# Performance work log

Measured on AMD Instinct MI355X. Metric: run time of the kernel, lower is better.

The kernel has to match this reference:

```python
import jax, jax.numpy as jnp
import numpy as np

B, S, IN, OUT = 4, 512, 1024, 512
T, G, K, R = 16, 2, 4, 32  # tables, groups, cells, rank
OUTPUT_SCALE = 1.0 / np.sqrt(T * G).astype(np.float32)


def setup_inputs() -> dict:
    key = jax.random.key(0)
    k0, k1, k2, k3 = jax.random.split(key, 4)
    x = jax.random.normal(k0, (B, S, IN), dtype=jnp.float32)
    proj_w = jax.random.normal(k1, (R, IN), dtype=jnp.float32) / np.sqrt(IN)
    router_w = jax.random.normal(k2, (T, G, K, R), dtype=jnp.float32) / np.sqrt(R)
    router_b = jnp.zeros((T, G, K), dtype=jnp.float32)
    affine_w = jax.random.normal(k3, (T, G, K, R, OUT), dtype=jnp.float32) * 0.02
    affine_b = jnp.zeros((T, G, K, OUT), dtype=jnp.float32)
    return {"x": x, "proj_w": proj_w, "router_w": router_w, "router_b": router_b,
            "affine_w": affine_w, "affine_b": affine_b}


def reference(x, proj_w, router_w, router_b, affine_w, affine_b):
    # z: (B,S,R) low-rank projection
    z = jnp.einsum('bsi,ri->bsr', x, proj_w)
    # routing scores per (table, group, cell): (B,S,T,G,K)
    scores = jnp.einsum('bsr,tgkr->bstgk', z, router_w) + router_b
    # per-cell affine outputs: (B,S,T,G,K,O) -- dominant intermediate
    cell_values = jnp.einsum('bsr,tgkro->bstgko', z, affine_w) + affine_b
    # tropical (min-plus) winner selection: argmin over cells
    winner = jnp.argmin(scores, axis=-1)  # (B,S,T,G)
    idx = jnp.broadcast_to(winner[..., None, None],
                           winner.shape + (1, cell_values.shape[-1]))
    group_output = jnp.take_along_axis(cell_values, idx, axis=4)[..., 0, :]  # (B,S,T,G,O)
    # sum over groups then tables, apply output scaling
    output = group_output.sum(axis=(2, 3)) * OUTPUT_SCALE  # (B,S,O)
    return output
```

## Files before the change

kernel.cpp:

```cpp
#include <hip/hip_runtime.h>

#define NTOK 2048
#define IN_DIM 1024
#define OUT_DIM 512
#define RNK 32
#define TG_N 32
#define TGK_N 128
#define AWCOLS 4096
#define KD 4224
#define NKT 66
#define SCALE_F 0.17677669529663687f

typedef __attribute__((ext_vector_type(8))) short short8;
typedef __attribute__((ext_vector_type(4))) float float4v;

__device__ __forceinline__ unsigned short f2bf(float f) {
  union { float f; unsigned int u; } c; c.f = f;
  unsigned int u = c.u;
  u += 0x7fffu + ((u >> 16) & 1u);
  return (unsigned short)(u >> 16);
}

__global__ __launch_bounds__(256) void k_w2t(
    const float* __restrict__ aw, const float* __restrict__ ab,
    unsigned short* __restrict__ w2t) {
  __shared__ float tile[32][33];
  const int c0 = blockIdx.x * 32, o0 = blockIdx.y * 32;
  const int t = threadIdx.x;
  const int oo = t & 31, cc = t >> 5;
#pragma unroll
  for (int p = 0; p < 4; ++p) {
    int cidx = c0 + cc + p * 8;
    float v = (cidx < AWCOLS)
                  ? aw[(size_t)cidx * OUT_DIM + o0 + oo]
                  : ab[(size_t)(cidx - AWCOLS) * OUT_DIM + o0 + oo];
    tile[cc + p * 8][oo] = v;
  }
  __syncthreads();
  if (t < 128) {
    const int ol = t >> 2, ch = t & 3;
    union { short8 v; unsigned short u[8]; } pk;
#pragma unroll
    for (int j = 0; j < 8; ++j) pk.u[j] = f2bf(tile[ch * 8 + j][ol]);
    *(short8*)(w2t + (size_t)(o0 + ol) * KD + c0 + ch * 8) = pk.v;
  }
}

__global__ __launch_bounds__(256) void k_zwin(
    const float* __restrict__ x, const float* __restrict__ proj_w,
    const float* __restrict__ router_w, const float* __restrict__ router_b,
    unsigned short* __restrict__ zout, unsigned long long* __restrict__ wout) {
  const int tok2 = blockIdx.x * 2;
  const int t = threadIdx.x;
  __shared__ __align__(16) float zbuf[2][RNK];
  __shared__ float sc[2][TGK_N];
  __shared__ int winbuf[2][TG_N];

  const int r = t >> 3, c = t & 7;
  const float4* w4 = (const float4*)(proj_w + (size_t)r * IN_DIM);
  const float4* x0 = (const float4*)(x + (size_t)tok2 * IN_DIM);
  float a0 = 0.f, a1 = 0.f;
#pragma unroll
  for (int jj = 0; jj < 32; ++jj) {
    float4 wv = w4[jj * 8 + c];
    float4 xv0 = x0[jj * 8 + c];
    float4 xv1 = x0[256 + jj * 8 + c];
    a0 += xv0.x * wv.x + xv0.y * wv.y + xv0.z * wv.z + xv0.w * wv.w;
    a1 += xv1.x * wv.x + xv1.y * wv.y + xv1.z * wv.z + xv1.w * wv.w;
  }
  a0 += __shfl_xor(a0, 1); a0 += __shfl_xor(a0, 2); a0 += __shfl_xor(a0, 4);
  a1 += __shfl_xor(a1, 1); a1 += __shfl_xor(a1, 2); a1 += __shfl_xor(a1, 4);
  if (c == 0) { zbuf[0][r] = a0; zbuf[1][r] = a1; }
  __syncthreads();

  {
    const int cell = t & 127, tk = t >> 7;
    const float4* rw = (const float4*)(router_w + (size_t)cell * RNK);
    const float4* zb = (const float4*)(&zbuf[tk][0]);
    float s = router_b[cell];
#pragma unroll
    for (int j = 0; j < 8; ++j) {
      float4 a = rw[j]; float4 b = zb[j];
      s += a.x * b.x + a.y * b.y + a.z * b.z + a.w * b.w;
    }
    sc[tk][cell] = s;
  }
  __syncthreads();

  if (t < 64) {
    const int tk = t >> 5, tg = t & 31;
    float best = sc[tk][tg * 4]; int w = 0;
#pragma unroll
    for (int k = 1; k < 4; ++k) {
      float v = sc[tk][tg * 4 + k];
      if (v < best) { best = v; w = k; }
    }
    winbuf[tk][tg] = w;
    zout[(size_t)(tok2 + tk) * RNK + tg] = f2bf(zbuf[tk][tg]);
  }
  __syncthreads();
  if (t < 2) {
    unsigned long long w = 0ull;
    for (int g = 0; g < TG_N; ++g)
      w |= ((unsigned long long)(winbuf[t][g] & 3)) << (2 * g);
    wout[tok2 + t] = w;
  }
}

__global__ __launch_bounds__(256) void k_gemm(
    const unsigned short* __restrict__ z, const unsigned long long* __restrict__ win,
    const unsigned short* __restrict__ Bt, float* __restrict__ out) {
  __shared__ __align__(16) unsigned short Bs[8][2048];
  const int blk = blockIdx.x;
  const int g = blk & 7, rest = blk >> 3;
  const int bn = g * 2 + (rest & 1);
  const int bm = rest >> 1;
  const int tid = threadIdx.x;
  const int wave = tid >> 6, lane = tid & 63;
  const int l15 = lane & 15, quad = lane >> 4;

  const int m0 = bm * 128 + wave * 32 + l15;
  const int m1 = m0 + 16;
  short8 z0 = *(const short8*)(z + (size_t)m0 * RNK + quad * 8);
  short8 z1 = *(const short8*)(z + (size_t)m1 * RNK + quad * 8);
  const unsigned long long w0 = win[m0], w1 = win[m1];

  const int sn = tid >> 3;
  const unsigned short* bsrc =
      Bt + (size_t)(bn * 32 + sn) * KD + (((tid & 7) ^ (sn & 7)) * 8);

  float4v acc00 = {}, acc01 = {}, acc10 = {}, acc11 = {};

#define ISSUE(KT)                                                                \
  __builtin_amdgcn_global_load_lds(                                              \
      (const __attribute__((address_space(1))) void*)(bsrc + (size_t)(KT) * 64), \
      (__attribute__((address_space(3))) void*)(&Bs[(KT) & 7][wave * 512]),      \
      16, 0, 0)

  auto compute = [&](int kt) __attribute__((always_inline)) {
    const unsigned short* sb = &Bs[kt & 7][0];
    const int fn0 = l15, fn1 = 16 + l15;
    if (kt < 64) {
      const int tg = kt >> 1;
      const unsigned e0 = (unsigned)(w0 >> (2 * tg)) & 3u;
      const unsigned e1 = (unsigned)(w1 >> (2 * tg)) & 3u;
#pragma unroll
      for (int s = 0; s < 2; ++s) {
        const unsigned kk = (unsigned)(((kt & 1) << 1) | s);
        short8 zz = {};
        short8 a0 = (e0 == kk) ? z0 : zz;
        short8 a1 = (e1 == kk) ? z1 : zz;
        short8 b0 = *(const short8*)(sb + fn0 * 64 + (((s * 4 + quad) ^ (fn0 & 7)) * 8));
        short8 b1 = *(const short8*)(sb + fn1 * 64 + (((s * 4 + quad) ^ (fn1 & 7)) * 8));
        acc00 = __builtin_amdgcn_mfma_f32_16x16x32_bf16(a0, b0, acc00, 0, 0, 0);
        acc01 = __builtin_amdgcn_mfma_f32_16x16x32_bf16(a0, b1, acc01, 0, 0, 0);
        acc10 = __builtin_amdgcn_mfma_f32_16x16x32_bf16(a1, b0, acc10, 0, 0, 0);
        acc11 = __builtin_amdgcn_mfma_f32_16x16x32_bf16(a1, b1, acc11, 0, 0, 0);
      }
    } else {
#pragma unroll
      for (int s = 0; s < 2; ++s) {
        const int tgA = (kt - 64) * 16 + s * 8 + quad * 2;
        union { short8 v; unsigned long long q[2]; } fa, fb;
        fa.q[0] = 0x3F80ull << (((unsigned)(w0 >> (2 * tgA)) & 3u) * 16);
        fa.q[1] = 0x3F80ull << (((unsigned)(w0 >> (2 * (tgA + 1))) & 3u) * 16);
        fb.q[0] = 0x3F80ull << (((unsigned)(w1 >> (2 * tgA)) & 3u) * 16);
        fb.q[1] = 0x3F80ull << (((unsigned)(w1 >> (2 * (tgA + 1))) & 3u) * 16);
        short8 b0 = *(const short8*)(sb + fn0 * 64 + (((s * 4 + quad) ^ (fn0 & 7)) * 8));
        short8 b1 = *(const short8*)(sb + fn1 * 64 + (((s * 4 + quad) ^ (fn1 & 7)) * 8));
        acc00 = __builtin_amdgcn_mfma_f32_16x16x32_bf16(fa.v, b0, acc00, 0, 0, 0);
        acc01 = __builtin_amdgcn_mfma_f32_16x16x32_bf16(fa.v, b1, acc01, 0, 0, 0);
        acc10 = __builtin_amdgcn_mfma_f32_16x16x32_bf16(fb.v, b0, acc10, 0, 0, 0);
        acc11 = __builtin_amdgcn_mfma_f32_16x16x32_bf16(fb.v, b1, acc11, 0, 0, 0);
      }
    }
  };

  ISSUE(0); ISSUE(1); ISSUE(2); ISSUE(3); ISSUE(4); ISSUE(5); ISSUE(6);

  for (int kt = 0; kt < 60; ++kt) {
    asm volatile("s_waitcnt vmcnt(6)" ::: "memory");
    asm volatile("s_barrier" ::: "memory");
    if (kt <= 58) ISSUE(kt + 7);
    compute(kt);
  }
  asm volatile("s_waitcnt vmcnt(5)" ::: "memory"); asm volatile("s_barrier" ::: "memory"); compute(60);
  asm volatile("s_waitcnt vmcnt(4)" ::: "memory"); asm volatile("s_barrier" ::: "memory"); compute(61);
  asm volatile("s_waitcnt vmcnt(3)" ::: "memory"); asm volatile("s_barrier" ::: "memory"); compute(62);
  asm volatile("s_waitcnt vmcnt(2)" ::: "memory"); asm volatile("s_barrier" ::: "memory"); compute(63);
  asm volatile("s_waitcnt vmcnt(1)" ::: "memory"); asm volatile("s_barrier" ::: "memory"); compute(64);
  asm volatile("s_waitcnt vmcnt(0)" ::: "memory"); asm volatile("s_barrier" ::: "memory"); compute(65);
#undef ISSUE

#pragma unroll
  for (int tm = 0; tm < 2; ++tm) {
#pragma unroll
    for (int tn = 0; tn < 2; ++tn) {
      float4v a = tm ? (tn ? acc11 : acc10) : (tn ? acc01 : acc00);
      const int col = bn * 32 + tn * 16 + l15;
      const int rowb = bm * 128 + wave * 32 + tm * 16 + quad * 4;
#pragma unroll
      for (int rg = 0; rg < 4; ++rg)
        out[(size_t)(rowb + rg) * OUT_DIM + col] = a[rg] * SCALE_F;
    }
  }
}

extern "C" void kernel_launch(void* const* d_in, const int* in_sizes, int n_in,
                              void* d_out, int out_size, void* d_ws, size_t ws_size,
                              hipStream_t stream) {
  const float* x        = (const float*)d_in[0];
  const float* proj_w   = (const float*)d_in[1];
  const float* router_w = (const float*)d_in[2];
  const float* router_b = (const float*)d_in[3];
  const float* affine_w = (const float*)d_in[4];
  const float* affine_b = (const float*)d_in[5];
  float* out = (float*)d_out;

  unsigned short* zout = (unsigned short*)d_ws;
  unsigned long long* wout = (unsigned long long*)((char*)d_ws + 131072);
  unsigned short* w2t = (unsigned short*)((char*)d_ws + 147456);

  k_w2t<<<dim3(KD / 32, OUT_DIM / 32), 256, 0, stream>>>(affine_w, affine_b, w2t);
  k_zwin<<<NTOK / 2, 256, 0, stream>>>(x, proj_w, router_w, router_b, zout, wout);
  k_gemm<<<256, 256, 0, stream>>>(zout, wout, w2t, out);
}
```

Measured before the change: 108.3 us.

## Fuse weight conversion, routing and GEMM into one persistent kernel with grid barrier

Merges the three kernels into a single 256-block launch. Each block first converts a strided share of affine weight tiles to bf16, then computes z and winners for 8 tokens, and waits at a global atomic barrier before running the existing MFMA GEMM. The aim is to remove two kernel launch gaps and the tail effects between dependent stages. In exchange it needs a memset per call, relies on all 256 blocks being co-resident, and runs the prep phases with fewer blocks and a larger LDS footprint per block.

```diff
diff --git a/kernel.cpp b/kernel.cpp
--- a/kernel.cpp
+++ b/kernel.cpp
@@ -21,115 +21,134 @@
   return (unsigned short)(u >> 16);
 }
 
-__global__ __launch_bounds__(256) void k_w2t(
+__global__ __launch_bounds__(256) void k_all(
     const float* __restrict__ aw, const float* __restrict__ ab,
-    unsigned short* __restrict__ w2t) {
-  __shared__ float tile[32][33];
-  const int c0 = blockIdx.x * 32, o0 = blockIdx.y * 32;
-  const int t = threadIdx.x;
-  const int oo = t & 31, cc = t >> 5;
-#pragma unroll
-  for (int p = 0; p < 4; ++p) {
-    int cidx = c0 + cc + p * 8;
-    float v = (cidx < AWCOLS)
-                  ? aw[(size_t)cidx * OUT_DIM + o0 + oo]
-                  : ab[(size_t)(cidx - AWCOLS) * OUT_DIM + o0 + oo];
-    tile[cc + p * 8][oo] = v;
-  }
-  __syncthreads();
-  if (t < 128) {
-    const int ol = t >> 2, ch = t & 3;
-    union { short8 v; unsigned short u[8]; } pk;
-#pragma unroll
-    for (int j = 0; j < 8; ++j) pk.u[j] = f2bf(tile[ch * 8 + j][ol]);
-    *(short8*)(w2t + (size_t)(o0 + ol) * KD + c0 + ch * 8) = pk.v;
-  }
-}
-
-__global__ __launch_bounds__(256) void k_zwin(
     const float* __restrict__ x, const float* __restrict__ proj_w,
     const float* __restrict__ router_w, const float* __restrict__ router_b,
-    unsigned short* __restrict__ zout, unsigned long long* __restrict__ wout) {
-  const int tok2 = blockIdx.x * 2;
+    unsigned short* __restrict__ w2t,
+    unsigned short* __restrict__ zout, unsigned long long* __restrict__ wout,
+    float* __restrict__ out, unsigned int* __restrict__ bar) {
   const int t = threadIdx.x;
-  __shared__ __align__(16) float zbuf[2][RNK];
-  __shared__ float sc[2][TGK_N];
-  __shared__ int winbuf[2][TG_N];
-
-  const int r = t >> 3, c = t & 7;
-  const float4* w4 = (const float4*)(proj_w + (size_t)r * IN_DIM);
-  const float4* x0 = (const float4*)(x + (size_t)tok2 * IN_DIM);
-  float a0 = 0.f, a1 = 0.f;
-#pragma unroll
-  for (int jj = 0; jj < 32; ++jj) {
-    float4 wv = w4[jj * 8 + c];
-    float4 xv0 = x0[jj * 8 + c];
-    float4 xv1 = x0[256 + jj * 8 + c];
-    a0 += xv0.x * wv.x + xv0.y * wv.y + xv0.z * wv.z + xv0.w * wv.w;
-    a1 += xv1.x * wv.x + xv1.y * wv.y + xv1.z * wv.z + xv1.w * wv.w;
-  }
-  a0 += __shfl_xor(a0, 1); a0 += __shfl_xor(a0, 2); a0 += __shfl_xor(a0, 4);
-  a1 += __shfl_xor(a1, 1); a1 += __shfl_xor(a1, 2); a1 += __shfl_xor(a1, 4);
-  if (c == 0) { zbuf[0][r] = a0; zbuf[1][r] = a1; }
+  const int blk = blockIdx.x;
+
+  __shared__ float tile[32][33];
+  __shared__ __align__(16) float zbuf[8][RNK];
+  __shared__ float sc[8][TGK_N];
+  __shared__ int winbuf[8][TG_N];
+  __shared__ __align__(16) unsigned short Bs[8][2048];
+
+  for (int tl = blk; tl < 2112; tl += 256) {
+    const int c0 = (tl % 132) * 32, o0 = (tl / 132) * 32;
+    const int oo = t & 31, cc = t >> 5;
+#pragma unroll
+    for (int p = 0; p < 4; ++p) {
+      int cidx = c0 + cc + p * 8;
+      float v = (cidx < AWCOLS)
+                    ? aw[(size_t)cidx * OUT_DIM + o0 + oo]
+                    : ab[(size_t)(cidx - AWCOLS) * OUT_DIM + o0 + oo];
+      tile[cc + p * 8][oo] = v;
+    }
+    __syncthreads();
+    if (t < 128) {
+      const int ol = t >> 2, ch = t & 3;
+      union { short8 v; unsigned short u[8]; } pk;
+#pragma unroll
+      for (int j = 0; j < 8; ++j) pk.u[j] = f2bf(tile[ch * 8 + j][ol]);
+      *(short8*)(w2t + (size_t)(o0 + ol) * KD + c0 + ch * 8) = pk.v;
+    }
+    __syncthreads();
+  }
+
+  {
+    const int tok8 = blk * 8;
+    const int r = t >> 3, c = t & 7;
+    const float4* w4 = (const float4*)(proj_w + (size_t)r * IN_DIM);
+    const float4* x0 = (const float4*)(x + (size_t)tok8 * IN_DIM);
+    float acc[8] = {};
+#pragma unroll
+    for (int jj = 0; jj < 32; ++jj) {
+      float4 wv = w4[jj * 8 + c];
+#pragma unroll
+      for (int tk = 0; tk < 8; ++tk) {
+        float4 xv = x0[tk * 256 + jj * 8 + c];
+        acc[tk] += xv.x * wv.x + xv.y * wv.y + xv.z * wv.z + xv.w * wv.w;
+      }
+    }
+#pragma unroll
+    for (int tk = 0; tk < 8; ++tk) {
+      float a = acc[tk];
+      a += __shfl_xor(a, 1); a += __shfl_xor(a, 2); a += __shfl_xor(a, 4);
+      if (c == 0) zbuf[tk][r] = a;
+    }
+    __syncthreads();
+    {
+      const int cell = t & 127, th = t >> 7;
+      const float4* rw = (const float4*)(router_w + (size_t)cell * RNK);
+      const float rb = router_b[cell];
+#pragma unroll
+      for (int p = 0; p < 4; ++p) {
+        const int tk = th + p * 2;
+        const float4* zb = (const float4*)(&zbuf[tk][0]);
+        float s = rb;
+#pragma unroll
+        for (int j = 0; j < 8; ++j) {
+          float4 a = rw[j]; float4 b = zb[j];
+          s += a.x * b.x + a.y * b.y + a.z * b.z + a.w * b.w;
+        }
+        sc[tk][cell] = s;
+      }
+    }
+    __syncthreads();
+    {
+      const int tk = t >> 5, tg = t & 31;
+      float best = sc[tk][tg * 4]; int w = 0;
+#pragma unroll
+      for (int k = 1; k < 4; ++k) {
+        float v = sc[tk][tg * 4 + k];
+        if (v < best) { best = v; w = k; }
+      }
+      winbuf[tk][tg] = w;
+      zout[(size_t)(tok8 + tk) * RNK + tg] = f2bf(zbuf[tk][tg]);
+    }
+    __syncthreads();
+    if (t < 8) {
+      unsigned long long w = 0ull;
+      for (int gg = 0; gg < TG_N; ++gg)
+        w |= ((unsigned long long)(winbuf[t][gg] & 3)) << (2 * gg);
+      wout[tok8 + t] = w;
+    }
+  }
+
   __syncthreads();
+  __threadfence();
+  if (t == 0) {
+    if (atomicAdd(&bar[0], 1u) == 255u) {
+      atomicExch(&bar[1], 1u);
+    } else {
+      while (atomicCAS(&bar[1], 9u, 9u) == 0u) __builtin_amdgcn_s_sleep(2);
+    }
+    __threadfence();
+  }
+  __syncthreads();
 
   {
-    const int cell = t & 127, tk = t >> 7;
-    const float4* rw = (const float4*)(router_w + (size_t)cell * RNK);
-    const float4* zb = (const float4*)(&zbuf[tk][0]);
-    float s = router_b[cell];
-#pragma unroll
-    for (int j = 0; j < 8; ++j) {
-      float4 a = rw[j]; float4 b = zb[j];
-      s += a.x * b.x + a.y * b.y + a.z * b.z + a.w * b.w;
-    }
-    sc[tk][cell] = s;
-  }
-  __syncthreads();
-
-  if (t < 64) {
-    const int tk = t >> 5, tg = t & 31;
-    float best = sc[tk][tg * 4]; int w = 0;
-#pragma unroll
-    for (int k = 1; k < 4; ++k) {
-      float v = sc[tk][tg * 4 + k];
-      if (v < best) { best = v; w = k; }
-    }
-    winbuf[tk][tg] = w;
-    zout[(size_t)(tok2 + tk) * RNK + tg] = f2bf(zbuf[tk][tg]);
-  }
-  __syncthreads();
-  if (t < 2) {
-    unsigned long long w = 0ull;
-    for (int g = 0; g < TG_N; ++g)
-      w |= ((unsigned long long)(winbuf[t][g] & 3)) << (2 * g);
-    wout[tok2 + t] = w;
-  }
-}
-
-__global__ __launch_bounds__(256) void k_gemm(
-    const unsigned short* __restrict__ z, const unsigned long long* __restrict__ win,
-    const unsigned short* __restrict__ Bt, float* __restrict__ out) {
-  __shared__ __align__(16) unsigned short Bs[8][2048];
-  const int blk = blockIdx.x;
-  const int g = blk & 7, rest = blk >> 3;
-  const int bn = g * 2 + (rest & 1);
-  const int bm = rest >> 1;
-  const int tid = threadIdx.x;
-  const int wave = tid >> 6, lane = tid & 63;
-  const int l15 = lane & 15, quad = lane >> 4;
-
-  const int m0 = bm * 128 + wave * 32 + l15;
-  const int m1 = m0 + 16;
-  short8 z0 = *(const short8*)(z + (size_t)m0 * RNK + quad * 8);
-  short8 z1 = *(const short8*)(z + (size_t)m1 * RNK + quad * 8);
-  const unsigned long long w0 = win[m0], w1 = win[m1];
-
-  const int sn = tid >> 3;
-  const unsigned short* bsrc =
-      Bt + (size_t)(bn * 32 + sn) * KD + (((tid & 7) ^ (sn & 7)) * 8);
-
-  float4v acc00 = {}, acc01 = {}, acc10 = {}, acc11 = {};
+    const int g = blk & 7, rest = blk >> 3;
+    const int bn = g * 2 + (rest & 1);
+    const int bm = rest >> 1;
+    const int wave = t >> 6, lane = t & 63;
+    const int l15 = lane & 15, quad = lane >> 4;
+
+    const int m0 = bm * 128 + wave * 32 + l15;
+    const int m1 = m0 + 16;
+    short8 z0 = *(const short8*)(zout + (size_t)m0 * RNK + quad * 8);
+    short8 z1 = *(const short8*)(zout + (size_t)m1 * RNK + quad * 8);
+    const unsigned long long w0 = wout[m0], w1 = wout[m1];
+
+    const int sn = t >> 3;
+    const unsigned short* bsrc =
+        w2t + (size_t)(bn * 32 + sn) * KD + (((t & 7) ^ (sn & 7)) * 8);
+
+    float4v acc00 = {}, acc01 = {}, acc10 = {}, acc11 = {};
 
 #define ISSUE(KT)                                                                \
   __builtin_amdgcn_global_load_lds(                                              \
@@ -137,71 +156,72 @@
       (__attribute__((address_space(3))) void*)(&Bs[(KT) & 7][wave * 512]),      \
       16, 0, 0)
 
-  auto compute = [&](int kt) __attribute__((always_inline)) {
-    const unsigned short* sb = &Bs[kt & 7][0];
-    const int fn0 = l15, fn1 = 16 + l15;
-    if (kt < 64) {
-      const int tg = kt >> 1;
-      const unsigned e0 = (unsigned)(w0 >> (2 * tg)) & 3u;
-      const unsigned e1 = (unsigned)(w1 >> (2 * tg)) & 3u;
-#pragma unroll
-      for (int s = 0; s < 2; ++s) {
-        const unsigned kk = (unsigned)(((kt & 1) << 1) | s);
-        short8 zz = {};
-        short8 a0 = (e0 == kk) ? z0 : zz;
-        short8 a1 = (e1 == kk) ? z1 : zz;
-        short8 b0 = *(const short8*)(sb + fn0 * 64 + (((s * 4 + quad) ^ (fn0 & 7)) * 8));
-        short8 b1 = *(const short8*)(sb + fn1 * 64 + (((s * 4 + quad) ^ (fn1 & 7)) * 8));
-        acc00 = __builtin_amdgcn_mfma_f32_16x16x32_bf16(a0, b0, acc00, 0, 0, 0);
-        acc01 = __builtin_amdgcn_mfma_f32_16x16x32_bf16(a0, b1, acc01, 0, 0, 0);
-        acc10 = __builtin_amdgcn_mfma_f32_16x16x32_bf16(a1, b0, acc10, 0, 0, 0);
-        acc11 = __builtin_amdgcn_mfma_f32_16x16x32_bf16(a1, b1, acc11, 0, 0, 0);
-      }
-    } else {
-#pragma unroll
-      for (int s = 0; s < 2; ++s) {
-        const int tgA = (kt - 64) * 16 + s * 8 + quad * 2;
-        union { short8 v; unsigned long long q[2]; } fa, fb;
-        fa.q[0] = 0x3F80ull << (((unsigned)(w0 >> (2 * tgA)) & 3u) * 16);
-        fa.q[1] = 0x3F80ull << (((unsigned)(w0 >> (2 * (tgA + 1))) & 3u) * 16);
-        fb.q[0] = 0x3F80ull << (((unsigned)(w1 >> (2 * tgA)) & 3u) * 16);
-        fb.q[1] = 0x3F80ull << (((unsigned)(w1 >> (2 * (tgA + 1))) & 3u) * 16);
-        short8 b0 = *(const short8*)(sb + fn0 * 64 + (((s * 4 + quad) ^ (fn0 & 7)) * 8));
-        short8 b1 = *(const short8*)(sb + fn1 * 64 + (((s * 4 + quad) ^ (fn1 & 7)) * 8));
-        acc00 = __builtin_amdgcn_mfma_f32_16x16x32_bf16(fa.v, b0, acc00, 0, 0, 0);
-        acc01 = __builtin_amdgcn_mfma_f32_16x16x32_bf16(fa.v, b1, acc01, 0, 0, 0);
-        acc10 = __builtin_amdgcn_mfma_f32_16x16x32_bf16(fb.v, b0, acc10, 0, 0, 0);
-        acc11 = __builtin_amdgcn_mfma_f32_16x16x32_bf16(fb.v, b1, acc11, 0, 0, 0);
-      }
-    }
-  };
-
-  ISSUE(0); ISSUE(1); ISSUE(2); ISSUE(3); ISSUE(4); ISSUE(5); ISSUE(6);
-
-  for (int kt = 0; kt < 60; ++kt) {
-    asm volatile("s_waitcnt vmcnt(6)" ::: "memory");
-    asm volatile("s_barrier" ::: "memory");
-    if (kt <= 58) ISSUE(kt + 7);
-    compute(kt);
-  }
-  asm volatile("s_waitcnt vmcnt(5)" ::: "memory"); asm volatile("s_barrier" ::: "memory"); compute(60);
-  asm volatile("s_waitcnt vmcnt(4)" ::: "memory"); asm volatile("s_barrier" ::: "memory"); compute(61);
-  asm volatile("s_waitcnt vmcnt(3)" ::: "memory"); asm volatile("s_barrier" ::: "memory"); compute(62);
-  asm volatile("s_waitcnt vmcnt(2)" ::: "memory"); asm volatile("s_barrier" ::: "memory"); compute(63);
-  asm volatile("s_waitcnt vmcnt(1)" ::: "memory"); asm volatile("s_barrier" ::: "memory"); compute(64);
-  asm volatile("s_waitcnt vmcnt(0)" ::: "memory"); asm volatile("s_barrier" ::: "memory"); compute(65);
+    auto compute = [&](int kt) __attribute__((always_inline)) {
+      const unsigned short* sb = &Bs[kt & 7][0];
+      const int fn0 = l15, fn1 = 16 + l15;
+      if (kt < 64) {
+        const int tg = kt >> 1;
+        const unsigned e0 = (unsigned)(w0 >> (2 * tg)) & 3u;
+        const unsigned e1 = (unsigned)(w1 >> (2 * tg)) & 3u;
+#pragma unroll
+        for (int s = 0; s < 2; ++s) {
+          const unsigned kk = (unsigned)(((kt & 1) << 1) | s);
+          short8 zz = {};
+          short8 a0 = (e0 == kk) ? z0 : zz;
+          short8 a1 = (e1 == kk) ? z1 : zz;
+          short8 b0 = *(const short8*)(sb + fn0 * 64 + (((s * 4 + quad) ^ (fn0 & 7)) * 8));
+          short8 b1 = *(const short8*)(sb + fn1 * 64 + (((s * 4 + quad) ^ (fn1 & 7)) * 8));
+          acc00 = __builtin_amdgcn_mfma_f32_16x16x32_bf16(a0, b0, acc00, 0, 0, 0);
+          acc01 = __builtin_amdgcn_mfma_f32_16x16x32_bf16(a0, b1, acc01, 0, 0, 0);
+          acc10 = __builtin_amdgcn_mfma_f32_16x16x32_bf16(a1, b0, acc10, 0, 0, 0);
+          acc11 = __builtin_amdgcn_mfma_f32_16x16x32_bf16(a1, b1, acc11, 0, 0, 0);
+        }
+      } else {
+#pragma unroll
+        for (int s = 0; s < 2; ++s) {
+          const int tgA = (kt - 64) * 16 + s * 8 + quad * 2;
+          union { short8 v; unsigned long long q[2]; } fa, fb;
+          fa.q[0] = 0x3F80ull << (((unsigned)(w0 >> (2 * tgA)) & 3u) * 16);
+          fa.q[1] = 0x3F80ull << (((unsigned)(w0 >> (2 * (tgA + 1))) & 3u) * 16);
+          fb.q[0] = 0x3F80ull << (((unsigned)(w1 >> (2 * tgA)) & 3u) * 16);
+          fb.q[1] = 0x3F80ull << (((unsigned)(w1 >> (2 * (tgA + 1))) & 3u) * 16);
+          short8 b0 = *(const short8*)(sb + fn0 * 64 + (((s * 4 + quad) ^ (fn0 & 7)) * 8));
+          short8 b1 = *(const short8*)(sb + fn1 * 64 + (((s * 4 + quad) ^ (fn1 & 7)) * 8));
+          acc00 = __builtin_amdgcn_mfma_f32_16x16x32_bf16(fa.v, b0, acc00, 0, 0, 0);
+          acc01 = __builtin_amdgcn_mfma_f32_16x16x32_bf16(fa.v, b1, acc01, 0, 0, 0);
+          acc10 = __builtin_amdgcn_mfma_f32_16x16x32_bf16(fb.v, b0, acc10, 0, 0, 0);
+          acc11 = __builtin_amdgcn_mfma_f32_16x16x32_bf16(fb.v, b1, acc11, 0, 0, 0);
+        }
+      }
+    };
+
+    ISSUE(0); ISSUE(1); ISSUE(2); ISSUE(3); ISSUE(4); ISSUE(5); ISSUE(6);
+
+    for (int kt = 0; kt < 60; ++kt) {
+      asm volatile("s_waitcnt vmcnt(6)" ::: "memory");
+      asm volatile("s_barrier" ::: "memory");
+      if (kt <= 58) ISSUE(kt + 7);
+      compute(kt);
+    }
+    asm volatile("s_waitcnt vmcnt(5)" ::: "memory"); asm volatile("s_barrier" ::: "memory"); compute(60);
+    asm volatile("s_waitcnt vmcnt(4)" ::: "memory"); asm volatile("s_barrier" ::: "memory"); compute(61);
+    asm volatile("s_waitcnt vmcnt(3)" ::: "memory"); asm volatile("s_barrier" ::: "memory"); compute(62);
+    asm volatile("s_waitcnt vmcnt(2)" ::: "memory"); asm volatile("s_barrier" ::: "memory"); compute(63);
+    asm volatile("s_waitcnt vmcnt(1)" ::: "memory"); asm volatile("s_barrier" ::: "memory"); compute(64);
+    asm volatile("s_waitcnt vmcnt(0)" ::: "memory"); asm volatile("s_barrier" ::: "memory"); compute(65);
 #undef ISSUE
 
 #pragma unroll
-  for (int tm = 0; tm < 2; ++tm) {
-#pragma unroll
-    for (int tn = 0; tn < 2; ++tn) {
-      float4v a = tm ? (tn ? acc11 : acc10) : (tn ? acc01 : acc00);
-      const int col = bn * 32 + tn * 16 + l15;
-      const int rowb = bm * 128 + wave * 32 + tm * 16 + quad * 4;
-#pragma unroll
-      for (int rg = 0; rg < 4; ++rg)
-        out[(size_t)(rowb + rg) * OUT_DIM + col] = a[rg] * SCALE_F;
+    for (int tm = 0; tm < 2; ++tm) {
+#pragma unroll
+      for (int tn = 0; tn < 2; ++tn) {
+        float4v a = tm ? (tn ? acc11 : acc10) : (tn ? acc01 : acc00);
+        const int col = bn * 32 + tn * 16 + l15;
+        const int rowb = bm * 128 + wave * 32 + tm * 16 + quad * 4;
+#pragma unroll
+        for (int rg = 0; rg < 4; ++rg)
+          out[(size_t)(rowb + rg) * OUT_DIM + col] = a[rg] * SCALE_F;
+      }
     }
   }
 }
@@ -220,8 +240,9 @@
   unsigned short* zout = (unsigned short*)d_ws;
   unsigned long long* wout = (unsigned long long*)((char*)d_ws + 131072);
   unsigned short* w2t = (unsigned short*)((char*)d_ws + 147456);
-
-  k_w2t<<<dim3(KD / 32, OUT_DIM / 32), 256, 0, stream>>>(affine_w, affine_b, w2t);
-  k_zwin<<<NTOK / 2, 256, 0, stream>>>(x, proj_w, router_w, router_b, zout, wout);
-  k_gemm<<<256, 256, 0, stream>>>(zout, wout, w2t, out);
+  unsigned int* bar = (unsigned int*)((char*)d_ws + 8388608);
+
+  hipMemsetAsync(bar, 0, 16, stream);
+  k_all<<<256, 256, 0, stream>>>(affine_w, affine_b, x, proj_w, router_w,
+                                 router_b, w2t, zout, wout, out, bar);
 }
```

Measured after the change: 276.6 us. +155.5%, slower.
